# Performance work log

Hardware: AMD Instinct MI355X
Metric: run time of the kernel (lower is better)

The kernel has to match this reference:

```python
import jax, jax.numpy as jnp
import numpy as np

DROPOUT_RATE = 0.25
STRIDE = 5  # must be odd


def setup_inputs() -> dict:
    key = jax.random.key(0)
    k1, k2 = jax.random.split(key)
    b, c, h, w = 4, 256, 64, 64
    x = jax.random.normal(k1, (b, c, h, w), dtype=jnp.float32)
    # uniform randoms underlying the dropout mask on the expanded grid
    rand_vals = jax.random.uniform(k2, (h * STRIDE, w * STRIDE), dtype=jnp.float32)
    return {"x": x, "rand_vals": rand_vals}


def reference(x, rand_vals):
    s = STRIDE
    s2 = s // 2
    rate = DROPOUT_RATE
    b, c, h, w = x.shape
    # zero-pad spatial dims by s//2 (ZeroPad2d)
    xp = jnp.pad(x, ((0, 0), (0, 0), (s2, s2), (s2, s2)))
    # x_new[:, :, i*s+p, j*s+q] = xp[:, :, i+p, j+q]  -> single fused gather
    idx_h = (jnp.arange(h)[:, None] + jnp.arange(s)[None, :]).reshape(h * s)  # [h*s]
    idx_w = (jnp.arange(w)[:, None] + jnp.arange(s)[None, :]).reshape(w * s)  # [w*s]
    x_new = xp[:, :, idx_h[:, None], idx_w[None, :]]  # [b, c, h*s, w*s]
    # dropout mask with forced keep at each patch center (s2 + i*s, s2 + j*s)
    mask = rand_vals > rate
    mask = mask.at[s2::s, s2::s].set(True)
    return x_new * mask.astype(x_new.dtype) / (1.0 - rate)
```

## Files before the change

### kernel.cpp

```cpp
#include <hip/hip_runtime.h>
#include <stdint.h>


#define KEEP_SCALE (1.0f / 0.75f)

__global__ __launch_bounds__(256) void build_mask_kernel(
    const float* __restrict__ rv,
    uint32_t* __restrict__ mask)
{
    int w = blockIdx.x * 256 + threadIdx.x;
    if (w >= 3200) return;
    int oh  = w / 10;
    int ow0 = (w - oh * 10) * 32;
    bool hc = (oh % 5) == 2;
    const float* rp = rv + oh * 320 + ow0;
    uint32_t m = 0;
    #pragma unroll
    for (int b = 0; b < 32; ++b) {
        int r = (ow0 + b) % 5;
        bool keep = (rp[b] > 0.25f) || (hc && r == 2);
        m |= (uint32_t)keep << b;
    }
    mask[w] = m;
}

__global__ __launch_bounds__(320) void expand_cps_dropout_kernel(
    const float* __restrict__ x,
    const uint32_t* __restrict__ mask,
    float* __restrict__ out)
{
    __shared__ float    xs[20 * 68];
    __shared__ uint32_t ms[640];

    const int t  = threadIdx.x;
    const int rg = blockIdx.x;
    const int bc = blockIdx.y;

    const int oh_blk  = rg * 64;
    const int ih_base = oh_blk / 5 - 2;
    const float* xi = x + (size_t)bc * 4096;

    for (int idx = t; idx < 20 * 68; idx += 320) {
        int sr = idx / 68;
        int c  = idx - sr * 68;
        int gih = ih_base + sr;
        int giw = c - 2;
        float v = 0.0f;
        if ((unsigned)gih < 64u && (unsigned)giw < 64u)
            v = xi[gih * 64 + giw];
        xs[idx] = v;
    }
    for (int idx = t; idx < 640; idx += 320)
        ms[idx] = mask[rg * 640 + idx];
    __syncthreads();

    const int ow4 = t % 80;
    const int ohL = t / 80;
    const int ow  = ow4 * 4;

    int iwp[4];
    #pragma unroll
    for (int k = 0; k < 4; ++k) {
        int o5 = ow + k;
        int q  = o5 / 5;
        int r  = o5 - q * 5;
        iwp[k] = q + r;
    }
    const int mw  = ow4 >> 3;
    const int msh = (ow4 & 7) * 4;

    float* op = out + (size_t)bc * 102400 + (size_t)(oh_blk + ohL) * 320 + ow;

    #pragma unroll
    for (int j = 0; j < 16; ++j) {
        int row = ohL + 4 * j;
        int ohg = oh_blk + row;
        int q   = ohg / 5;
        int r   = ohg - q * 5;
        int sr  = q + r - 2 - ih_base;
        const float* xr = xs + sr * 68;
        uint32_t mb = ms[row * 10 + mw] >> msh;

        float4 o;
        o.x = (mb & 1u) ? xr[iwp[0]] * KEEP_SCALE : 0.0f;
        o.y = (mb & 2u) ? xr[iwp[1]] * KEEP_SCALE : 0.0f;
        o.z = (mb & 4u) ? xr[iwp[2]] * KEEP_SCALE : 0.0f;
        o.w = (mb & 8u) ? xr[iwp[3]] * KEEP_SCALE : 0.0f;
        *reinterpret_cast<float4*>(op + (size_t)(4 * j) * 320) = o;
    }
}

extern "C" void kernel_launch(void* const* d_in, const int* in_sizes, int n_in,
                              void* d_out, int out_size, void* d_ws, size_t ws_size,
                              hipStream_t stream) {
    const float* x  = (const float*)d_in[0];
    const float* rv = (const float*)d_in[1];
    float* out      = (float*)d_out;
    uint32_t* mask  = (uint32_t*)d_ws;

    hipLaunchKernelGGL(build_mask_kernel, dim3(13), dim3(256), 0, stream, rv, mask);

    dim3 block(320);
    dim3 grid(5, 1024);
    hipLaunchKernelGGL(expand_cps_dropout_kernel, grid, block, 0, stream,
                       x, mask, out);
}
```

Baseline: 97.33 us.

## Fold padding into mask, use direct global-to-LDS loads and nontemporal stores

Folds the zero-padding condition into the precomputed bitmask so the main kernel can stage unpadded input rows straight into LDS with global_load_lds, with no bounds checks. Each block now covers half of a channel's output (160 rows) instead of 64 rows, so there are fewer, larger blocks and less redundant halo loading. Output is written with nontemporal vector stores to avoid polluting the cache with streaming data. The risk is lower occupancy and parallelism from only 2048 blocks, and the longer loop per thread.

```diff
diff --git a/kernel.cpp b/kernel.cpp
--- a/kernel.cpp
+++ b/kernel.cpp
@@ -3,6 +3,8 @@
 
 
 #define KEEP_SCALE (1.0f / 0.75f)
+
+typedef float f32x4 __attribute__((ext_vector_type(4)));
 
 __global__ __launch_bounds__(256) void build_mask_kernel(
     const float* __restrict__ rv,
@@ -12,13 +14,19 @@
     if (w >= 3200) return;
     int oh  = w / 10;
     int ow0 = (w - oh * 10) * 32;
-    bool hc = (oh % 5) == 2;
+    int qh = oh / 5, rh = oh - qh * 5;
+    int ih = qh + rh - 2;
+    bool hok = ((unsigned)ih < 64u);
+    bool hc  = (rh == 2);
     const float* rp = rv + oh * 320 + ow0;
     uint32_t m = 0;
     #pragma unroll
     for (int b = 0; b < 32; ++b) {
-        int r = (ow0 + b) % 5;
-        bool keep = (rp[b] > 0.25f) || (hc && r == 2);
+        int ow = ow0 + b;
+        int q = ow / 5, r = ow - q * 5;
+        int iw = q + r - 2;
+        bool keep = ((rp[b] > 0.25f) || (hc && (r == 2)))
+                    && hok && ((unsigned)iw < 64u);
         m |= (uint32_t)keep << b;
     }
     mask[w] = m;
@@ -29,64 +37,65 @@
     const uint32_t* __restrict__ mask,
     float* __restrict__ out)
 {
-    __shared__ float    xs[20 * 68];
-    __shared__ uint32_t ms[640];
+    __shared__ float    xs[34 * 64];
+    __shared__ uint32_t ms[1600];
 
-    const int t  = threadIdx.x;
-    const int rg = blockIdx.x;
-    const int bc = blockIdx.y;
+    const int t    = threadIdx.x;
+    const int half = blockIdx.x;
+    const int bc   = blockIdx.y;
+    const int r0   = half ? 30 : 0;
 
-    const int oh_blk  = rg * 64;
-    const int ih_base = oh_blk / 5 - 2;
-    const float* xi = x + (size_t)bc * 4096;
-
-    for (int idx = t; idx < 20 * 68; idx += 320) {
-        int sr = idx / 68;
-        int c  = idx - sr * 68;
-        int gih = ih_base + sr;
-        int giw = c - 2;
-        float v = 0.0f;
-        if ((unsigned)gih < 64u && (unsigned)giw < 64u)
-            v = xi[gih * 64 + giw];
-        xs[idx] = v;
+    const float* xsrc = x + (size_t)bc * 4096 + r0 * 64;
+    for (int i = t; i < 544; i += 320) {
+        __builtin_amdgcn_global_load_lds(
+            (const __attribute__((address_space(1))) void*)(xsrc + i * 4),
+            (__attribute__((address_space(3))) void*)(xs + (i & ~63) * 4),
+            16, 0, 0);
     }
-    for (int idx = t; idx < 640; idx += 320)
-        ms[idx] = mask[rg * 640 + idx];
+    const uint32_t* msrc = mask + half * 1600;
+    for (int i = t; i < 400; i += 320) {
+        __builtin_amdgcn_global_load_lds(
+            (const __attribute__((address_space(1))) void*)(msrc + i * 4),
+            (__attribute__((address_space(3))) void*)(ms + (i & ~63) * 4),
+            16, 0, 0);
+    }
     __syncthreads();
 
     const int ow4 = t % 80;
     const int ohL = t / 80;
     const int ow  = ow4 * 4;
 
-    int iwp[4];
+    int xoffb[4];
     #pragma unroll
     for (int k = 0; k < 4; ++k) {
-        int o5 = ow + k;
-        int q  = o5 / 5;
-        int r  = o5 - q * 5;
-        iwp[k] = q + r;
+        int o = ow + k;
+        int q = o / 5, r = o - q * 5;
+        int iw = q + r - 2;
+        iw = iw < 0 ? 0 : (iw > 63 ? 63 : iw);
+        xoffb[k] = iw * 4;
     }
-    const int mw  = ow4 >> 3;
     const int msh = (ow4 & 7) * 4;
+    const uint32_t* msp = ms + ohL * 10 + (ow4 >> 3);
+    const char* xsb = (const char*)xs;
 
-    float* op = out + (size_t)bc * 102400 + (size_t)(oh_blk + ohL) * 320 + ow;
+    float* op = out + (size_t)bc * 102400 + (size_t)(half * 160 + ohL) * 320 + ow;
+    const int ohbase = half * 160 + ohL;
 
-    #pragma unroll
-    for (int j = 0; j < 16; ++j) {
-        int row = ohL + 4 * j;
-        int ohg = oh_blk + row;
-        int q   = ohg / 5;
-        int r   = ohg - q * 5;
-        int sr  = q + r - 2 - ih_base;
-        const float* xr = xs + sr * 68;
-        uint32_t mb = ms[row * 10 + mw] >> msh;
+    #pragma unroll 8
+    for (int j = 0; j < 40; ++j) {
+        int oh = ohbase + 4 * j;
+        int q = oh / 5, r = oh - q * 5;
+        int ih = q + r - 2;
+        ih = ih < 0 ? 0 : (ih > 63 ? 63 : ih);
+        const char* xr = xsb + (ih - r0) * 256;
+        uint32_t mb = msp[j * 40] >> msh;
 
-        float4 o;
-        o.x = (mb & 1u) ? xr[iwp[0]] * KEEP_SCALE : 0.0f;
-        o.y = (mb & 2u) ? xr[iwp[1]] * KEEP_SCALE : 0.0f;
-        o.z = (mb & 4u) ? xr[iwp[2]] * KEEP_SCALE : 0.0f;
-        o.w = (mb & 8u) ? xr[iwp[3]] * KEEP_SCALE : 0.0f;
-        *reinterpret_cast<float4*>(op + (size_t)(4 * j) * 320) = o;
+        f32x4 o;
+        o.x = (mb & 1u) ? *(const float*)(xr + xoffb[0]) * KEEP_SCALE : 0.0f;
+        o.y = (mb & 2u) ? *(const float*)(xr + xoffb[1]) * KEEP_SCALE : 0.0f;
+        o.z = (mb & 4u) ? *(const float*)(xr + xoffb[2]) * KEEP_SCALE : 0.0f;
+        o.w = (mb & 8u) ? *(const float*)(xr + xoffb[3]) * KEEP_SCALE : 0.0f;
+        __builtin_nontemporal_store(o, (f32x4*)(op + (size_t)(4 * j) * 320));
     }
 }
 
@@ -101,7 +110,7 @@
     hipLaunchKernelGGL(build_mask_kernel, dim3(13), dim3(256), 0, stream, rv, mask);
 
     dim3 block(320);
-    dim3 grid(5, 1024);
+    dim3 grid(2, 1024);
     hipLaunchKernelGGL(expand_cps_dropout_kernel, grid, block, 0, stream,
                        x, mask, out);
 }
```

After: 100.9 us. 1.04x slower.
